# Kernel tuning notes

Measured on AMD Instinct MI355X. Metric: run time of the kernel, lower is better.

## Reference

```python
import jax, jax.numpy as jnp
import numpy as np

BATCH, IN_DIM, UNITS = 2048, 512, 512


def setup_inputs() -> dict:
    key = jax.random.key(0)
    k1, k2 = jax.random.split(key)
    x = jax.random.normal(k1, (BATCH, IN_DIM), dtype=jnp.float32)
    # He-style init for W, shape (1, in_dim, units) as in build()
    W = jax.random.normal(k2, (1, IN_DIM, UNITS), dtype=jnp.float32) * np.float32(np.sqrt(2.0 / IN_DIM))
    bias = jnp.zeros((UNITS,), dtype=jnp.float32)
    return {"x": x, "W": W, "bias": bias}


def reference(x, W, bias):
    # nodal 'exponential': exp(x * w) - 1, broadcast (batch,in,1)*(1,in,units)
    z = jnp.exp(x[:, :, None] * W) - 1.0          # (batch, in, units)
    # pool 'maximum': reduce over input dim
    p = jnp.max(z, axis=1)                         # (batch, units)
    # bias add + activation 'tanh'
    return jnp.tanh(p + bias)
```

## Files before the change

kernel.cpp:

```cpp
#include <hip/hip_runtime.h>


#define BATCH 2048
#define INDIM 512
#define UNITS 512

#define KC 32
#define RB 32
#define RGRP 16
#define NW 16

typedef float v2f __attribute__((ext_vector_type(2)));

__global__ __launch_bounds__(1024, 8) void maxexp_kernel(
    const float* __restrict__ x,
    const float* __restrict__ W,
    const float* __restrict__ bias,
    float* __restrict__ out)
{
    __shared__ float part[RGRP][NW][64];

    const int f    = blockIdx.x;
    const int band = (f & 7) * 8 + ((f >> 3) & 7);
    const int ut   = f >> 6;

    const int lane = threadIdx.x & 63;
    const int wv   = __builtin_amdgcn_readfirstlane(threadIdx.x >> 6);
    const int u    = ut * 64 + lane;
    const int k0   = wv * KC;
    const int b0   = band * RB;

    v2f wp[KC / 2];
    {
        const float* wb = W + (size_t)k0 * UNITS + u;
#pragma unroll
        for (int j = 0; j < KC / 2; ++j) {
            v2f t;
            t.x = wb[(size_t)(2 * j)     * UNITS];
            t.y = wb[(size_t)(2 * j + 1) * UNITS];
            wp[j] = t;
        }
    }
#pragma unroll
    for (int j = 0; j < KC / 2; ++j) asm("" : "+v"(wp[j]));

    const float bv = bias[u];
    const float* xb = x + (size_t)b0 * INDIM + k0;

#pragma unroll 1
    for (int g = 0; g < RB / RGRP; ++g) {
        const float* xg = xb + (size_t)g * RGRP * INDIM;

#pragma unroll
        for (int rr = 0; rr < RGRP; ++rr) {
            const v2f* xr = reinterpret_cast<const v2f*>(xg + (size_t)rr * INDIM);
            float m0 = -3.4e38f, m1 = -3.4e38f;
#pragma unroll
            for (int j = 0; j < KC / 2; j += 2) {
                v2f p0, p1;
                asm("v_pk_mul_f32 %0, %1, %2" : "=v"(p0) : "s"(xr[j]),     "v"(wp[j]));
                asm("v_pk_mul_f32 %0, %1, %2" : "=v"(p1) : "s"(xr[j + 1]), "v"(wp[j + 1]));
                m0 = fmaxf(fmaxf(m0, p0.x), p0.y);
                m1 = fmaxf(fmaxf(m1, p1.x), p1.y);
            }
            part[rr][wv][lane] = fmaxf(m0, m1);
        }

        __syncthreads();

        {
            float m = -3.4e38f;
#pragma unroll
            for (int j = 0; j < NW; j += 2)
                m = fmaxf(fmaxf(m, part[wv][j][lane]), part[wv][j + 1][lane]);
            const float pp = __expf(m) - 1.0f + bv;
            const float e  = __expf(2.0f * pp);
            out[(size_t)(b0 + g * RGRP + wv) * UNITS + u] = 1.0f - 2.0f / (e + 1.0f);
        }

        __syncthreads();
    }
}

extern "C" void kernel_launch(void* const* d_in, const int* in_sizes, int n_in,
                              void* d_out, int out_size, void* d_ws, size_t ws_size,
                              hipStream_t stream) {
    const float* x    = (const float*)d_in[0];
    const float* W    = (const float*)d_in[1];
    const float* bias = (const float*)d_in[2];
    float* out = (float*)d_out;

    dim3 grid(512);
    dim3 block(1024);
    maxexp_kernel<<<grid, block, 0, stream>>>(x, W, bias, out);
}
```

Before: 27.87 us.

## Stream W tiles through double-buffered LDS and accumulate full K per wave

Replaces the split-K design, in which each wave held a 32-row slice of W in registers and partial maxima were reduced through shared memory, with a design where each block covers a 128-unit by 16-row tile. W chunks are streamed into double-buffered LDS with global_load_lds while x rows are read as scalar-uniform vectors. Each lane accumulates a 2x2 register tile over the full K. This removes the cross-wave partial reduction and the barriers per row group, at the cost of repeated LDS reads of W and a barrier per K chunk.

```diff
diff --git a/kernel.cpp b/kernel.cpp
--- a/kernel.cpp
+++ b/kernel.cpp
@@ -5,81 +5,100 @@
 #define INDIM 512
 #define UNITS 512
 
-#define KC 32
-#define RB 32
-#define RGRP 16
-#define NW 16
+#define BK  32
+#define UT  128
+#define RPW 2
+#define NW  8
 
-typedef float v2f __attribute__((ext_vector_type(2)));
+typedef float f16v __attribute__((ext_vector_type(16)));
 
-__global__ __launch_bounds__(1024, 8) void maxexp_kernel(
+__global__ __launch_bounds__(512, 4) void maxexp_kernel(
     const float* __restrict__ x,
     const float* __restrict__ W,
     const float* __restrict__ bias,
     float* __restrict__ out)
 {
-    __shared__ float part[RGRP][NW][64];
+    __shared__ float wlds[2][BK][UT];
 
     const int f    = blockIdx.x;
-    const int band = (f & 7) * 8 + ((f >> 3) & 7);
-    const int ut   = f >> 6;
+    const int g    = (f & 7) * 64 + (f >> 3);
+    const int ut   = g & 3;
+    const int rowg = g >> 2;
+    const int u0   = ut * UT;
+    const int b0   = rowg * (NW * RPW);
 
-    const int lane = threadIdx.x & 63;
-    const int wv   = __builtin_amdgcn_readfirstlane(threadIdx.x >> 6);
-    const int u    = ut * 64 + lane;
-    const int k0   = wv * KC;
-    const int b0   = band * RB;
+    const int tid  = threadIdx.x;
+    const int lane = tid & 63;
+    const int wv   = __builtin_amdgcn_readfirstlane(tid >> 6);
 
-    v2f wp[KC / 2];
-    {
-        const float* wb = W + (size_t)k0 * UNITS + u;
-#pragma unroll
-        for (int j = 0; j < KC / 2; ++j) {
-            v2f t;
-            t.x = wb[(size_t)(2 * j)     * UNITS];
-            t.y = wb[(size_t)(2 * j + 1) * UNITS];
-            wp[j] = t;
-        }
+    const float* xr0 = x + (size_t)(b0 + 2 * wv)     * INDIM;
+    const float* xr1 = x + (size_t)(b0 + 2 * wv + 1) * INDIM;
+
+#define STAGE(buf_, c_)                                                        \
+    {                                                                          \
+        _Pragma("unroll")                                                      \
+        for (int j = 0; j < 2; ++j) {                                          \
+            const int kr = 4 * wv + 2 * j;                                     \
+            const float* src_ = W + (size_t)((c_) * BK + kr + (lane >> 5)) * UNITS \
+                                + u0 + 4 * (lane & 31);                        \
+            __builtin_amdgcn_global_load_lds(                                  \
+                (const __attribute__((address_space(1))) unsigned int*)src_,   \
+                (__attribute__((address_space(3))) unsigned int*)&wlds[buf_][kr][0], \
+                16, 0, 0);                                                     \
+        }                                                                      \
     }
-#pragma unroll
-    for (int j = 0; j < KC / 2; ++j) asm("" : "+v"(wp[j]));
 
-    const float bv = bias[u];
-    const float* xb = x + (size_t)b0 * INDIM + k0;
+    float a00 = -3.4e38f, a01 = -3.4e38f, a10 = -3.4e38f, a11 = -3.4e38f;
 
+    STAGE(0, 0);
+    __syncthreads();
+
+    const int NCH = INDIM / BK;
 #pragma unroll 1
-    for (int g = 0; g < RB / RGRP; ++g) {
-        const float* xg = xb + (size_t)g * RGRP * INDIM;
+    for (int c = 0; c < NCH; ++c) {
+        const int buf = c & 1;
+        if (c + 1 < NCH) STAGE(buf ^ 1, c + 1);
+
+        const f16v x0a = *reinterpret_cast<const f16v*>(xr0 + c * BK);
+        const f16v x0b = *reinterpret_cast<const f16v*>(xr0 + c * BK + 16);
+        const f16v x1a = *reinterpret_cast<const f16v*>(xr1 + c * BK);
+        const f16v x1b = *reinterpret_cast<const f16v*>(xr1 + c * BK + 16);
 
 #pragma unroll
-        for (int rr = 0; rr < RGRP; ++rr) {
-            const v2f* xr = reinterpret_cast<const v2f*>(xg + (size_t)rr * INDIM);
-            float m0 = -3.4e38f, m1 = -3.4e38f;
-#pragma unroll
-            for (int j = 0; j < KC / 2; j += 2) {
-                v2f p0, p1;
-                asm("v_pk_mul_f32 %0, %1, %2" : "=v"(p0) : "s"(xr[j]),     "v"(wp[j]));
-                asm("v_pk_mul_f32 %0, %1, %2" : "=v"(p1) : "s"(xr[j + 1]), "v"(wp[j + 1]));
-                m0 = fmaxf(fmaxf(m0, p0.x), p0.y);
-                m1 = fmaxf(fmaxf(m1, p1.x), p1.y);
-            }
-            part[rr][wv][lane] = fmaxf(m0, m1);
-        }
-
-        __syncthreads();
-
-        {
-            float m = -3.4e38f;
-#pragma unroll
-            for (int j = 0; j < NW; j += 2)
-                m = fmaxf(fmaxf(m, part[wv][j][lane]), part[wv][j + 1][lane]);
-            const float pp = __expf(m) - 1.0f + bv;
-            const float e  = __expf(2.0f * pp);
-            out[(size_t)(b0 + g * RGRP + wv) * UNITS + u] = 1.0f - 2.0f / (e + 1.0f);
+        for (int kp = 0; kp < BK / 2; ++kp) {
+            const float2 wA = *reinterpret_cast<const float2*>(&wlds[buf][2 * kp][2 * lane]);
+            const float2 wB = *reinterpret_cast<const float2*>(&wlds[buf][2 * kp + 1][2 * lane]);
+            const float xe0 = (kp < 8) ? x0a[(2 * kp) & 15]     : x0b[(2 * kp) & 15];
+            const float xo0 = (kp < 8) ? x0a[(2 * kp + 1) & 15] : x0b[(2 * kp + 1) & 15];
+            const float xe1 = (kp < 8) ? x1a[(2 * kp) & 15]     : x1b[(2 * kp) & 15];
+            const float xo1 = (kp < 8) ? x1a[(2 * kp + 1) & 15] : x1b[(2 * kp + 1) & 15];
+            a00 = fmaxf(fmaxf(a00, xe0 * wA.x), xo0 * wB.x);
+            a01 = fmaxf(fmaxf(a01, xe0 * wA.y), xo0 * wB.y);
+            a10 = fmaxf(fmaxf(a10, xe1 * wA.x), xo1 * wB.x);
+            a11 = fmaxf(fmaxf(a11, xe1 * wA.y), xo1 * wB.y);
         }
 
         __syncthreads();
     }
+
+    const float2 bv = *reinterpret_cast<const float2*>(bias + u0 + 2 * lane);
+    {
+        const float p0 = __expf(a00) - 1.0f + bv.x;
+        const float p1 = __expf(a01) - 1.0f + bv.y;
+        float2 o;
+        o.x = 1.0f - 2.0f / (__expf(2.0f * p0) + 1.0f);
+        o.y = 1.0f - 2.0f / (__expf(2.0f * p1) + 1.0f);
+        *reinterpret_cast<float2*>(out + (size_t)(b0 + 2 * wv) * UNITS + u0 + 2 * lane) = o;
+    }
+    {
+        const float p0 = __expf(a10) - 1.0f + bv.x;
+        const float p1 = __expf(a11) - 1.0f + bv.y;
+        float2 o;
+        o.x = 1.0f - 2.0f / (__expf(2.0f * p0) + 1.0f);
+        o.y = 1.0f - 2.0f / (__expf(2.0f * p1) + 1.0f);
+        *reinterpret_cast<float2*>(out + (size_t)(b0 + 2 * wv + 1) * UNITS + u0 + 2 * lane) = o;
+    }
+#undef STAGE
 }
 
 extern "C" void kernel_launch(void* const* d_in, const int* in_sizes, int n_in,
@@ -91,6 +110,6 @@
     float* out = (float*)d_out;
 
     dim3 grid(512);
-    dim3 block(1024);
+    dim3 block(512);
     maxexp_kernel<<<grid, block, 0, stream>>>(x, W, bias, out);
 }
```

Result: slower. 29.31 us (+5.1%).
